# Kernel tuning notes

Measured on AMD Instinct MI355X. Metric: run time of the kernel, lower is better.

Reference implementation:

```python
import jax, jax.numpy as jnp
import numpy as np
from jax import ops

N, E, B = 50000, 800000, 64      # nodes, edges, graphs in the batch
D_RAW, D_NAMES = 48, 16          # raw node feats + name embedding -> concat = 64
HID, HEADS = 64, 4               # hidden_dim, num_heads


def setup_inputs() -> dict:
    key = jax.random.key(0)
    ks = iter(jax.random.split(key, 48))
    nrm = lambda shape, s=0.05: jax.random.normal(next(ks), shape, jnp.float32) * s
    inp = dict(
        nfeats=nrm((N, D_RAW), 1.0),
        names=nrm((N, D_NAMES), 1.0),
        centrality=jax.random.uniform(next(ks), (N, 1), jnp.float32) + 0.5,
        edge_weight=jax.random.uniform(next(ks), (E,), jnp.float32),
        src=jax.random.randint(next(ks), (E,), 0, N),
        dst=jax.random.randint(next(ks), (E,), 0, N),
        gid=jnp.sort(jax.random.randint(next(ks), (N,), 0, B)),
    )
    for l in (1, 2, 3):  # three GATConv layers (all in_feats == HID)
        inp[f'W{l}'] = nrm((HID, HEADS * HID))
        inp[f'al{l}'] = nrm((HEADS, HID))
        inp[f'ar{l}'] = nrm((HEADS, HID))
        inp[f'b{l}'] = jnp.zeros((HEADS * HID,), jnp.float32)
    for l in (0, 1, 2, 3):  # four GlobalAttentionPooling gate nets
        inp[f'Wg{l}'] = nrm((HID, 1))
        inp[f'bg{l}'] = jnp.zeros((1,), jnp.float32)
    inp['Wih'] = nrm((4 * HID, HID))
    inp['Whh'] = nrm((4 * HID, HID))
    inp['bih'] = jnp.zeros((4 * HID,), jnp.float32)
    inp['bhh'] = jnp.zeros((4 * HID,), jnp.float32)
    inp['Wc'] = nrm((HID, 1))
    inp['bc'] = jnp.zeros((1,), jnp.float32)
    return inp


def _seg_softmax(e, idx, n):
    """Numerically stable softmax of e over segments given by idx."""
    m = ops.segment_max(e, idx, num_segments=n)
    ex = jnp.exp(e - m[idx])
    s = ops.segment_sum(ex, idx, num_segments=n)
    return ex / s[idx]


def _gat(x, W, al, ar, b, src, dst, ew):
    """DGL GATConv with edge_weight: softmax over incoming edges per dst,
    edge_weight multiplied AFTER the softmax (DGL semantics), bias added."""
    n = x.shape[0]
    ft = (x @ W).reshape(n, HEADS, HID)                 # [N,H,D]
    el = jnp.einsum('nhd,hd->nh', ft, al)
    er = jnp.einsum('nhd,hd->nh', ft, ar)
    e = jax.nn.leaky_relu(el[src] + er[dst], 0.2)       # [E,H]
    a = _seg_softmax(e, dst, n) * ew[:, None]           # [E,H]
    rst = ops.segment_sum(a[:, :, None] * ft[src], dst, num_segments=n)
    return rst + b.reshape(1, HEADS, HID)               # [N,H,D]


def _gap(x, Wg, bg, gid):
    """GlobalAttentionPooling: per-graph softmax gate, weighted node sum."""
    gate = _seg_softmax(x @ Wg + bg, gid, B)            # [N,1]
    return ops.segment_sum(gate * x, gid, num_segments=B)  # [B,D]


def _lstm(xs, Wih, Whh, bih, bhh):
    h = jnp.zeros((xs.shape[1], HID), xs.dtype)
    c = h
    def step(carry, x):
        h, c = carry
        g = x @ Wih.T + bih + h @ Whh.T + bhh
        i, f, gg, o = jnp.split(g, 4, axis=-1)          # torch gate order i,f,g,o
        c = jax.nn.sigmoid(f) * c + jax.nn.sigmoid(i) * jnp.tanh(gg)
        h = jax.nn.sigmoid(o) * jnp.tanh(c)
        return (h, c), h
    (h, _), _ = jax.lax.scan(step, (h, c), xs)
    return h                                            # last hidden state [B,D]


def reference(nfeats, names, centrality, edge_weight, src, dst, gid,
              W1, al1, ar1, b1, W2, al2, ar2, b2, W3, al3, ar3, b3,
              Wg0, bg0, Wg1, bg1, Wg2, bg2, Wg3, bg3,
              Wih, Whh, bih, bhh, Wc, bc):
    x = jnp.concatenate((nfeats, names), axis=1) * centrality
    hg0 = _gap(x, Wg0, bg0, gid)
    h = jax.nn.relu(_gat(x, W1, al1, ar1, b1, src, dst, edge_weight)).mean(axis=1)
    hg1 = _gap(h, Wg1, bg1, gid)
    h = jax.nn.relu(_gat(h, W2, al2, ar2, b2, src, dst, edge_weight)).mean(axis=1)
    hg2 = _gap(h, Wg2, bg2, gid)
    h = jax.nn.relu(_gat(h, W3, al3, ar3, b3, src, dst, edge_weight)).mean(axis=1)
    hg3 = _gap(h, Wg3, bg3, gid)
    seq = jnp.stack((hg0, hg1, hg2, hg3), axis=0)       # [4,B,D]
    hT = _lstm(seq, Wih, Whh, bih, bhh)                 # [B,D]
    return jax.nn.sigmoid(hT @ Wc + bc)                 # [B,1]
```

## Files before the change

### kernel.cpp

```cpp
#include <hip/hip_runtime.h>
#include <hip/hip_bf16.h>

#define N_NODES 50000
#define N_EDGES 800000
#define N_GRAPHS 64
#define SCAN_B 196
#define FT_B   3125
#define GAP_B  512
#define G1     784
#define EPB    1024

typedef unsigned short u16;
typedef unsigned char u8;
typedef unsigned int u32;
typedef short s16x8 __attribute__((ext_vector_type(8)));
typedef float f32x4 __attribute__((ext_vector_type(4)));
typedef float f32x2 __attribute__((ext_vector_type(2)));

__device__ __forceinline__ float bf2f(u16 u) {
    union { unsigned int i; float f; } v; v.i = ((unsigned int)u) << 16; return v.f;
}
__device__ __forceinline__ u16 f2bf(float f) {
    union { float f; unsigned int i; } v; v.f = f;
    unsigned int i = v.i;
    unsigned int r = i + 0x7fffu + ((i >> 16) & 1u);
    return (u16)(r >> 16);
}
__device__ __forceinline__ float asfloat(unsigned int u) {
    union { unsigned int i; float f; } v; v.i = u; return v.f;
}

__global__ __launch_bounds__(256) void k_init(const float* __restrict__ nf, const float* __restrict__ nm,
                                              const float* __restrict__ cent, const float* __restrict__ Wg,
                                              const float* __restrict__ bg,
                                              u16* __restrict__ x, float* __restrict__ g) {
    int node = blockIdx.x * 4 + (threadIdx.x >> 6);
    int lane = threadIdx.x & 63;
    float v = (lane < 48) ? nf[(size_t)node * 48 + lane] : nm[(size_t)node * 16 + lane - 48];
    float xf = v * cent[node];
    x[(size_t)node * 64 + lane] = f2bf(xf);
    float p = xf * Wg[lane];
#pragma unroll
    for (int mm = 1; mm < 64; mm <<= 1) p += __shfl_xor(p, mm);
    if (lane == 0) g[node] = p + bg[0];
}

__global__ __launch_bounds__(256) void k_bin1(const int* __restrict__ src, const int* __restrict__ dst,
                                              const float* __restrict__ ew,
                                              u32* __restrict__ bedge, u8* __restrict__ bdlo,
                                              int* __restrict__ runstart) {
    int s = blockIdx.x, t = threadIdx.x;
    int e0 = s * EPB;
    int n = N_EDGES - e0; if (n > EPB) n = EPB; if (n < 0) n = 0;
    __shared__ int lcnt[256];
    __shared__ int lcur[256];
    __shared__ int wsum[4];
    lcnt[t] = 0;
    __syncthreads();
    for (int i = t; i < n; i += 256) atomicAdd(&lcnt[dst[e0 + i] >> 8], 1);
    __syncthreads();
    int v = lcnt[t], orig = v;
    int lane = t & 63, w = t >> 6;
#pragma unroll
    for (int d = 1; d < 64; d <<= 1) {
        int u = __shfl_up(v, d);
        if (lane >= d) v += u;
    }
    if (lane == 63) wsum[w] = v;
    __syncthreads();
    int add = 0;
    for (int k = 0; k < w; k++) add += wsum[k];
    v += add;
    int excl = v - orig;
    if (t < SCAN_B) runstart[s * 197 + t] = excl;
    if (t == 255) runstart[s * 197 + 196] = v;
    lcur[t] = excl;
    __syncthreads();
    for (int i = t; i < n; i += 256) {
        int d = dst[e0 + i];
        int pos = atomicAdd(&lcur[d >> 8], 1);
        bedge[e0 + pos] = ((u32)f2bf(ew[e0 + i]) << 16) | (u32)src[e0 + i];
        bdlo[e0 + pos] = (u8)(d & 255);
    }
}

__global__ __launch_bounds__(256) void k_cntscan(const int* __restrict__ runstart, const u8* __restrict__ bdlo,
                                                 int* __restrict__ rowptr, int* __restrict__ bsum) {
    int b = blockIdx.x, t = threadIdx.x;
    __shared__ int ndeg[256];
    __shared__ int wsum[4];
    ndeg[t] = 0;
    __syncthreads();
    for (int s = t; s < G1; s += 256) {
        int rs = runstart[s * 197 + b], re = runstart[s * 197 + b + 1];
        const u8* p = bdlo + (size_t)s * EPB;
        for (int i = rs; i < re; i++) atomicAdd(&ndeg[p[i]], 1);
    }
    __syncthreads();
    int v = ndeg[t], orig = v;
    int lane = t & 63, w = t >> 6;
#pragma unroll
    for (int d = 1; d < 64; d <<= 1) {
        int u = __shfl_up(v, d);
        if (lane >= d) v += u;
    }
    if (lane == 63) wsum[w] = v;
    __syncthreads();
    int add = 0;
    for (int k = 0; k < w; k++) add += wsum[k];
    v += add;
    int node = b * 256 + t;
    if (node < N_NODES) rowptr[node] = v - orig;
    if (t == 255) bsum[b] = v;
}

__global__ __launch_bounds__(256) void k_scanBprep(const int* __restrict__ bsum, int* __restrict__ boff,
                                                   int* __restrict__ rowptr,
                                                   const float* __restrict__ W1, const float* __restrict__ W2,
                                                   const float* __restrict__ W3, u16* __restrict__ Wt) {
    __shared__ float tile[64][65];
    __shared__ int wsum[4];
    if (blockIdx.x == 0) {
        int t = threadIdx.x;
        int v = (t < SCAN_B) ? bsum[t] : 0;
        int orig = v;
        int lane = t & 63, w = t >> 6;
#pragma unroll
        for (int d = 1; d < 64; d <<= 1) {
            int u = __shfl_up(v, d);
            if (lane >= d) v += u;
        }
        if (lane == 63) wsum[w] = v;
        __syncthreads();
        int add = 0;
        for (int k = 0; k < w; k++) add += wsum[k];
        v += add;
        if (t < SCAN_B) boff[t] = v - orig;
        if (t == 0) rowptr[N_NODES] = N_EDGES;
        return;
    }
    int bb = blockIdx.x - 1;
    int l = bb >> 2, ti = bb & 3;
    const float* W = (l == 0) ? W1 : (l == 1) ? W2 : W3;
    u16* o = Wt + (size_t)l * 64 * 256;
    int t = threadIdx.x;
    for (int i = t; i < 64 * 64; i += 256) {
        int d = i >> 6, c = i & 63;
        tile[d][c] = W[d * 256 + ti * 64 + c];
    }
    __syncthreads();
    for (int i = t; i < 64 * 64; i += 256) {
        int c = i >> 6, d = i & 63;
        o[(size_t)(ti * 64 + c) * 64 + d] = f2bf(tile[d][c]);
    }
}

__global__ __launch_bounds__(256) void k_csr2(int* __restrict__ rowptr, const int* __restrict__ boff,
                                              const int* __restrict__ runstart, const u32* __restrict__ bedge,
                                              const u8* __restrict__ bdlo, u32* __restrict__ csr_se) {
    int b = blockIdx.x, t = threadIdx.x;
    __shared__ int cur[256];
    int node = b * 256 + t;
    if (node < N_NODES) {
        int val = rowptr[node] + boff[b];
        rowptr[node] = val;
        cur[t] = val;
    } else cur[t] = 0;
    __syncthreads();
    for (int s = t; s < G1; s += 256) {
        int rs = runstart[s * 197 + b], re = runstart[s * 197 + b + 1];
        const u32* pe = bedge + (size_t)s * EPB;
        const u8* pd = bdlo + (size_t)s * EPB;
        for (int i = rs; i < re; i++) {
            int pos = atomicAdd(&cur[pd[i]], 1);
            csr_se[pos] = pe[i];
        }
    }
}

__device__ __forceinline__ void gap_part(int pb, const u16* __restrict__ x, const float* __restrict__ g,
                                         const int* __restrict__ gid,
                                         float* __restrict__ pnum, float* __restrict__ pden) {
    int part = pb & 7, b = pb >> 3;
    int t = threadIdx.x, w = t >> 6, lane = t & 63, q = lane >> 4, c = lane & 15;
    int lo = 0, hi = N_NODES;
    while (lo < hi) { int mid = (lo + hi) >> 1; if (gid[mid] < b) lo = mid + 1; else hi = mid; }
    int s = lo;
    lo = 0; hi = N_NODES;
    while (lo < hi) { int mid = (lo + hi) >> 1; if (gid[mid] < b + 1) lo = mid + 1; else hi = mid; }
    int e = lo;
    int len = e - s;
    int ps = s + (int)(((long long)len * part) >> 3);
    int pe = s + (int)(((long long)len * (part + 1)) >> 3);

    float a0 = 0.f, a1 = 0.f, a2 = 0.f, a3 = 0.f, den = 0.f;
    for (int n0 = ps + w * 4; n0 < pe; n0 += 16) {
        int node = n0 + q;
        if (node < pe) {
            float gate = __expf(fminf(g[node], 30.f));
            uint2 raw = *(const uint2*)(x + (size_t)node * 64 + c * 4);
            a0 = fmaf(gate, asfloat(raw.x << 16), a0);
            a1 = fmaf(gate, asfloat(raw.x & 0xffff0000u), a1);
            a2 = fmaf(gate, asfloat(raw.y << 16), a2);
            a3 = fmaf(gate, asfloat(raw.y & 0xffff0000u), a3);
            if (c == 0) den += gate;
        }
    }
#pragma unroll
    for (int mm = 16; mm < 64; mm <<= 1) {
        a0 += __shfl_xor(a0, mm); a1 += __shfl_xor(a1, mm);
        a2 += __shfl_xor(a2, mm); a3 += __shfl_xor(a3, mm);
        den += __shfl_xor(den, mm);
    }
    __shared__ float snum[4][64];
    __shared__ float sden[4];
    if (lane < 16) {
        snum[w][c * 4 + 0] = a0; snum[w][c * 4 + 1] = a1;
        snum[w][c * 4 + 2] = a2; snum[w][c * 4 + 3] = a3;
        if (lane == 0) sden[w] = den;
    }
    __syncthreads();
    if (t < 64) pnum[((size_t)b * 8 + part) * 64 + t] = snum[0][t] + snum[1][t] + snum[2][t] + snum[3][t];
    if (t == 0) pden[b * 8 + part] = sden[0] + sden[1] + sden[2] + sden[3];
}

__global__ __launch_bounds__(256) void k_ftgap(const u16* __restrict__ X, const u16* __restrict__ Wt,
                                               const float* __restrict__ al, const float* __restrict__ ar,
                                               u8* __restrict__ ft, float* __restrict__ el, float* __restrict__ er,
                                               const float* __restrict__ g, const int* __restrict__ gid,
                                               float* __restrict__ pnum, float* __restrict__ pden) {
    if (blockIdx.x >= FT_B) {
        gap_part(blockIdx.x - FT_B, X, g, gid, pnum, pden);
        return;
    }
    int w = threadIdx.x >> 6;
    int lane = threadIdx.x & 63;
    int quad = lane >> 4, c = lane & 15;
    int n0 = blockIdx.x * 16;

    f32x4 acc[4];
#pragma unroll
    for (int t = 0; t < 4; t++) acc[t] = (f32x4){0.f, 0.f, 0.f, 0.f};

#pragma unroll
    for (int kh = 0; kh < 2; kh++) {
        s16x8 a = *(const s16x8*)(X + (size_t)(n0 + c) * 64 + kh * 32 + quad * 8);
#pragma unroll
        for (int t = 0; t < 4; t++) {
            int col = w * 64 + t * 16 + c;
            s16x8 b = *(const s16x8*)(Wt + (size_t)col * 64 + kh * 32 + quad * 8);
            acc[t] = __builtin_amdgcn_mfma_f32_16x16x32_bf16(a, b, acc[t], 0, 0, 0);
        }
    }

    __shared__ u8 sft[16 * 256];
    float alv[4], arv[4];
#pragma unroll
    for (int t = 0; t < 4; t++) {
        alv[t] = al[w * 64 + t * 16 + c];
        arv[t] = ar[w * 64 + t * 16 + c];
    }
    float pel[4] = {0.f, 0.f, 0.f, 0.f}, per[4] = {0.f, 0.f, 0.f, 0.f};
#pragma unroll
    for (int t = 0; t < 4; t++) {
#pragma unroll
        for (int r = 0; r < 4; r++) {
            float v = acc[t][r];
            int nl = quad * 4 + r;
            int d = t * 16 + c;
            int pk = __builtin_amdgcn_cvt_pk_fp8_f32(v, v, 0, false);
            sft[nl * 256 + d * 4 + w] = (u8)(pk & 0xff);
            pel[r] += v * alv[t];
            per[r] += v * arv[t];
        }
    }
#pragma unroll
    for (int r = 0; r < 4; r++) {
#pragma unroll
        for (int mm = 1; mm < 16; mm <<= 1) {
            pel[r] += __shfl_xor(pel[r], mm);
            per[r] += __shfl_xor(per[r], mm);
        }
    }
    if (c == 0) {
#pragma unroll
        for (int r = 0; r < 4; r++) {
            int node = n0 + quad * 4 + r;
            el[node * 4 + w] = pel[r];
            er[node * 4 + w] = per[r];
        }
    }
    __syncthreads();
    const uint4* s4 = (const uint4*)sft;
    uint4* g4 = (uint4*)(ft + (size_t)n0 * 256);
    g4[threadIdx.x] = s4[threadIdx.x];
}

__global__ __launch_bounds__(256) void k_agg(
    const u8* __restrict__ ft, const float4* __restrict__ el4, const float4* __restrict__ er4,
    const int* __restrict__ rowptr, const u32* __restrict__ csr_se,
    const float* __restrict__ bias, const float* __restrict__ Wg, const float* __restrict__ bg,
    u16* __restrict__ hout, float* __restrict__ gout) {
    int wv = threadIdx.x >> 6;
    int node = blockIdx.x * 4 + wv;
    int lane = threadIdx.x & 63;
    int beg = rowptr[node], end = rowptr[node + 1];
    float4 erv = er4[node];

    __shared__ int    s_off[4][64];
    __shared__ float4 s_p[4][64];

    float S0 = 0.f, S1 = 0.f, S2 = 0.f, S3 = 0.f;
    float a0 = 0.f, a1 = 0.f, a2 = 0.f, a3 = 0.f;

    const char* ftl = (const char*)ft + lane * 4;

    for (int base = beg; base < end; base += 64) {
        int cnt = end - base; if (cnt > 64) cnt = 64;
        if (lane < cnt) {
            u32 se = csr_se[base + lane];
            int sidx = (int)(se & 0xffffu);
            float w = bf2f((u16)(se >> 16));
            float4 elv = el4[sidx];
            float t0 = elv.x + erv.x, t1 = elv.y + erv.y, t2 = elv.z + erv.z, t3 = elv.w + erv.w;
            t0 = t0 > 0.f ? t0 : 0.2f * t0;
            t1 = t1 > 0.f ? t1 : 0.2f * t1;
            t2 = t2 > 0.f ? t2 : 0.2f * t2;
            t3 = t3 > 0.f ? t3 : 0.2f * t3;
            float p0 = __expf(fminf(t0, 30.f));
            float p1 = __expf(fminf(t1, 30.f));
            float p2 = __expf(fminf(t2, 30.f));
            float p3 = __expf(fminf(t3, 30.f));
            S0 += p0; S1 += p1; S2 += p2; S3 += p3;
            s_off[wv][lane] = sidx * 256;
            s_p[wv][lane] = make_float4(p0 * w, p1 * w, p2 * w, p3 * w);
        }
        int k = 0;
        for (; k + 4 <= cnt; k += 4) {
            int o0 = s_off[wv][k], o1 = s_off[wv][k + 1], o2 = s_off[wv][k + 2], o3 = s_off[wv][k + 3];
            unsigned r0 = *(const unsigned*)(ftl + o0);
            unsigned r1 = *(const unsigned*)(ftl + o1);
            unsigned r2 = *(const unsigned*)(ftl + o2);
            unsigned r3 = *(const unsigned*)(ftl + o3);
            float4 q0 = s_p[wv][k], q1 = s_p[wv][k + 1], q2 = s_p[wv][k + 2], q3 = s_p[wv][k + 3];
            f32x2 l0 = __builtin_amdgcn_cvt_pk_f32_fp8(r0, false), h0 = __builtin_amdgcn_cvt_pk_f32_fp8(r0, true);
            f32x2 l1 = __builtin_amdgcn_cvt_pk_f32_fp8(r1, false), h1 = __builtin_amdgcn_cvt_pk_f32_fp8(r1, true);
            f32x2 l2 = __builtin_amdgcn_cvt_pk_f32_fp8(r2, false), h2 = __builtin_amdgcn_cvt_pk_f32_fp8(r2, true);
            f32x2 l3 = __builtin_amdgcn_cvt_pk_f32_fp8(r3, false), h3 = __builtin_amdgcn_cvt_pk_f32_fp8(r3, true);
            a0 = fmaf(q0.x, l0.x, a0); a1 = fmaf(q0.y, l0.y, a1);
            a2 = fmaf(q0.z, h0.x, a2); a3 = fmaf(q0.w, h0.y, a3);
            a0 = fmaf(q1.x, l1.x, a0); a1 = fmaf(q1.y, l1.y, a1);
            a2 = fmaf(q1.z, h1.x, a2); a3 = fmaf(q1.w, h1.y, a3);
            a0 = fmaf(q2.x, l2.x, a0); a1 = fmaf(q2.y, l2.y, a1);
            a2 = fmaf(q2.z, h2.x, a2); a3 = fmaf(q2.w, h2.y, a3);
            a0 = fmaf(q3.x, l3.x, a0); a1 = fmaf(q3.y, l3.y, a1);
            a2 = fmaf(q3.z, h3.x, a2); a3 = fmaf(q3.w, h3.y, a3);
        }
        for (; k < cnt; k++) {
            int o0 = s_off[wv][k];
            float4 q0 = s_p[wv][k];
            unsigned r0 = *(const unsigned*)(ftl + o0);
            f32x2 l0 = __builtin_amdgcn_cvt_pk_f32_fp8(r0, false), h0 = __builtin_amdgcn_cvt_pk_f32_fp8(r0, true);
            a0 = fmaf(q0.x, l0.x, a0); a1 = fmaf(q0.y, l0.y, a1);
            a2 = fmaf(q0.z, h0.x, a2); a3 = fmaf(q0.w, h0.y, a3);
        }
    }
#pragma unroll
    for (int mm = 1; mm < 64; mm <<= 1) {
        S0 += __shfl_xor(S0, mm);
        S1 += __shfl_xor(S1, mm);
        S2 += __shfl_xor(S2, mm);
        S3 += __shfl_xor(S3, mm);
    }
    float i0 = S0 > 0.f ? 1.f / S0 : 0.f;
    float i1 = S1 > 0.f ? 1.f / S1 : 0.f;
    float i2 = S2 > 0.f ? 1.f / S2 : 0.f;
    float i3 = S3 > 0.f ? 1.f / S3 : 0.f;
    float r0 = a0 * i0 + bias[lane];
    float r1 = a1 * i1 + bias[64 + lane];
    float r2 = a2 * i2 + bias[128 + lane];
    float r3 = a3 * i3 + bias[192 + lane];
    float o = (fmaxf(r0, 0.f) + fmaxf(r1, 0.f) + fmaxf(r2, 0.f) + fmaxf(r3, 0.f)) * 0.25f;
    hout[(size_t)node * 64 + lane] = f2bf(o);
    float pg = o * Wg[lane];
#pragma unroll
    for (int mm = 1; mm < 64; mm <<= 1) pg += __shfl_xor(pg, mm);
    if (lane == 0) gout[node] = pg + bg[0];
}

__global__ __launch_bounds__(256) void k_gapP(const u16* __restrict__ x, const float* __restrict__ g,
                                              const int* __restrict__ gid,
                                              float* __restrict__ pnum, float* __restrict__ pden) {
    gap_part(blockIdx.x, x, g, gid, pnum, pden);
}

__global__ __launch_bounds__(256) void k_lstm(const float* __restrict__ pnum, const float* __restrict__ pden,
                                              const float* __restrict__ Wih, const float* __restrict__ Whh,
                                              const float* __restrict__ bih, const float* __restrict__ bhh,
                                              const float* __restrict__ Wc, const float* __restrict__ bc,
                                              float* __restrict__ out) {
    int b = blockIdx.x, t = threadIdx.x;
    __shared__ float h[64], c[64], G[256], xv[64], red[64];
    if (t < 64) { h[t] = 0.f; c[t] = 0.f; }
    __syncthreads();
    for (int step = 0; step < 4; step++) {
        if (t < 64) {
            const float* pn = pnum + (((size_t)step * N_GRAPHS + b) * 8) * 64;
            const float* pd = pden + ((size_t)step * N_GRAPHS + b) * 8;
            float num = 0.f, dn = 0.f;
#pragma unroll
            for (int pp = 0; pp < 8; pp++) { num += pn[pp * 64 + t]; dn += pd[pp]; }
            xv[t] = (dn > 0.f) ? num / dn : 0.f;
        }
        __syncthreads();
        float acc = bih[t] + bhh[t];
#pragma unroll 4
        for (int d = 0; d < 64; d++)
            acc += xv[d] * Wih[t * 64 + d] + h[d] * Whh[t * 64 + d];
        G[t] = acc;
        __syncthreads();
        if (t < 64) {
            float ig = 1.f / (1.f + __expf(-G[t]));
            float fg = 1.f / (1.f + __expf(-G[64 + t]));
            float gg = tanhf(G[128 + t]);
            float og = 1.f / (1.f + __expf(-G[192 + t]));
            float cn = fg * c[t] + ig * gg;
            c[t] = cn;
            h[t] = og * tanhf(cn);
        }
        __syncthreads();
    }
    if (t < 64) red[t] = h[t] * Wc[t];
    __syncthreads();
    if (t == 0) {
        float r = 0.f;
        for (int i = 0; i < 64; i++) r += red[i];
        r += bc[0];
        out[b] = 1.f / (1.f + __expf(-r));
    }
}

extern "C" void kernel_launch(void* const* d_in, const int* in_sizes, int n_in,
                              void* d_out, int out_size, void* d_ws, size_t ws_size,
                              hipStream_t stream) {
    const float* nf   = (const float*)d_in[0];
    const float* nm   = (const float*)d_in[1];
    const float* cent = (const float*)d_in[2];
    const float* ew   = (const float*)d_in[3];
    const int* src  = (const int*)d_in[4];
    const int* dst  = (const int*)d_in[5];
    const int* gid  = (const int*)d_in[6];
    const float* W[3]  = {(const float*)d_in[7],  (const float*)d_in[11], (const float*)d_in[15]};
    const float* al[3] = {(const float*)d_in[8],  (const float*)d_in[12], (const float*)d_in[16]};
    const float* ar[3] = {(const float*)d_in[9],  (const float*)d_in[13], (const float*)d_in[17]};
    const float* bb[3] = {(const float*)d_in[10], (const float*)d_in[14], (const float*)d_in[18]};
    const float* Wg[4] = {(const float*)d_in[19], (const float*)d_in[21], (const float*)d_in[23], (const float*)d_in[25]};
    const float* bg[4] = {(const float*)d_in[20], (const float*)d_in[22], (const float*)d_in[24], (const float*)d_in[26]};
    const float* Wih = (const float*)d_in[27];
    const float* Whh = (const float*)d_in[28];
    const float* bih = (const float*)d_in[29];
    const float* bhh = (const float*)d_in[30];
    const float* Wc  = (const float*)d_in[31];
    const float* bc  = (const float*)d_in[32];
    float* out = (float*)d_out;

    char* p = (char*)d_ws;
    size_t off = 0;
    auto A = [&](size_t bytes) -> char* {
        char* r = p + off;
        off += (bytes + 255) & ~(size_t)255;
        return r;
    };
    u8*    ftb     = (u8*)   A((size_t)N_NODES * 256);
    u16*   nodebuf = (u16*)  A((size_t)N_NODES * 64 * 2);
    u32*   csr_se  = (u32*)  A((size_t)N_EDGES * 4);
    u32*   bedge   = (u32*)  A((size_t)G1 * EPB * 4);
    u8*    bdlo    = (u8*)   A((size_t)G1 * EPB);
    int*   runstart= (int*)  A((size_t)G1 * 197 * 4);
    float* el      = (float*)A((size_t)N_NODES * 4 * 4);
    float* er      = (float*)A((size_t)N_NODES * 4 * 4);
    float* gbuf    = (float*)A((size_t)N_NODES * 4);
    int*   rowptr  = (int*)  A((size_t)(N_NODES + 1) * 4);
    float* pnum    = (float*)A((size_t)4 * N_GRAPHS * 8 * 64 * 4);
    float* pden    = (float*)A((size_t)4 * N_GRAPHS * 8 * 4);
    int*   bsum    = (int*)  A((size_t)SCAN_B * 4);
    int*   boff    = (int*)  A((size_t)SCAN_B * 4);
    u16*   Wt      = (u16*)  A((size_t)3 * 64 * 256 * 2);

    k_init<<<N_NODES / 4, 256, 0, stream>>>(nf, nm, cent, Wg[0], bg[0], nodebuf, gbuf);
    k_bin1<<<G1, 256, 0, stream>>>(src, dst, ew, bedge, bdlo, runstart);
    k_cntscan<<<SCAN_B, 256, 0, stream>>>(runstart, bdlo, rowptr, bsum);
    k_scanBprep<<<13, 256, 0, stream>>>(bsum, boff, rowptr, W[0], W[1], W[2], Wt);
    k_csr2<<<SCAN_B, 256, 0, stream>>>(rowptr, boff, runstart, bedge, bdlo, csr_se);

    for (int l = 0; l < 3; l++) {
        k_ftgap<<<FT_B + GAP_B, 256, 0, stream>>>(nodebuf, Wt + (size_t)l * 64 * 256, al[l], ar[l],
                                                  ftb, el, er, gbuf, gid,
                                                  pnum + (size_t)l * N_GRAPHS * 8 * 64,
                                                  pden + (size_t)l * N_GRAPHS * 8);
        k_agg<<<N_NODES / 4, 256, 0, stream>>>(ftb, (const float4*)el, (const float4*)er, rowptr,
                                               csr_se, bb[l], Wg[l + 1], bg[l + 1], nodebuf, gbuf);
    }
    k_gapP<<<GAP_B, 256, 0, stream>>>(nodebuf, gbuf, gid,
                                      pnum + (size_t)3 * N_GRAPHS * 8 * 64,
                                      pden + (size_t)3 * N_GRAPHS * 8);
    k_lstm<<<N_GRAPHS, 256, 0, stream>>>(pnum, pden, Wih, Whh, bih, bhh, Wc, bc, out);
}
```

Measured before the change: 388.5 us.

## Aggregate raw node features before projection and fold attention vectors into weights

Uses linearity to reorder each GAT layer. Edges now aggregate 64-dim fp8 node inputs with per-head weights, and the 64x256 projection runs afterwards on the aggregated [N,256] result in a fused MFMA GEMM that also applies bias, relu, head mean, gate and next-layer el/er. This shrinks the gathered row from 256 bytes to 64 bytes, and el/er come from precomputed W·al and W·ar vectors. It also merges edge binning with weight prep and writes a bf16 [N,256] intermediate, which adds extra memory traffic and per-lane byte gathers.

```diff
diff --git a/kernel.cpp b/kernel.cpp
--- a/kernel.cpp
+++ b/kernel.cpp
@@ -5,7 +5,8 @@
 #define N_EDGES 800000
 #define N_GRAPHS 64
 #define SCAN_B 196
-#define FT_B   3125
+#define AGG_B  12500
+#define GEMM_B 3125
 #define GAP_B  512
 #define G1     784
 #define EPB    1024
@@ -29,58 +30,132 @@
 __device__ __forceinline__ float asfloat(unsigned int u) {
     union { unsigned int i; float f; } v; v.i = u; return v.f;
 }
+__device__ __forceinline__ u8 f2fp8(float f) {
+    int pk = __builtin_amdgcn_cvt_pk_fp8_f32(f, f, 0, false);
+    return (u8)(pk & 0xff);
+}
+__device__ __forceinline__ float fp82f(u32 b) {
+    f32x2 v = __builtin_amdgcn_cvt_pk_f32_fp8(b, false);
+    return v.x;
+}
+
+__global__ __launch_bounds__(256) void k_binprep(
+    const int* __restrict__ src, const int* __restrict__ dst, const float* __restrict__ ew,
+    u32* __restrict__ bedge, u8* __restrict__ bdlo, int* __restrict__ runstart,
+    const float* __restrict__ W1, const float* __restrict__ W2, const float* __restrict__ W3,
+    const float* __restrict__ al1, const float* __restrict__ al2, const float* __restrict__ al3,
+    const float* __restrict__ ar1, const float* __restrict__ ar2, const float* __restrict__ ar3,
+    const float* __restrict__ Wg0, const float* __restrict__ Wg1,
+    const float* __restrict__ Wg2, const float* __restrict__ Wg3,
+    u16* __restrict__ Wt, float* __restrict__ U) {
+    __shared__ float tile[64][65];
+    __shared__ int lcnt[256];
+    __shared__ int lcur[256];
+    __shared__ int wsum[4];
+    int t = threadIdx.x;
+    if (blockIdx.x < G1) {
+        int s = blockIdx.x;
+        int e0 = s * EPB;
+        int n = N_EDGES - e0; if (n > EPB) n = EPB; if (n < 0) n = 0;
+        lcnt[t] = 0;
+        __syncthreads();
+        for (int i = t; i < n; i += 256) atomicAdd(&lcnt[dst[e0 + i] >> 8], 1);
+        __syncthreads();
+        int v = lcnt[t], orig = v;
+        int lane = t & 63, w = t >> 6;
+#pragma unroll
+        for (int d = 1; d < 64; d <<= 1) {
+            int u = __shfl_up(v, d);
+            if (lane >= d) v += u;
+        }
+        if (lane == 63) wsum[w] = v;
+        __syncthreads();
+        int add = 0;
+        for (int k = 0; k < w; k++) add += wsum[k];
+        v += add;
+        int excl = v - orig;
+        if (t < SCAN_B) runstart[s * 197 + t] = excl;
+        if (t == 255) runstart[s * 197 + 196] = v;
+        lcur[t] = excl;
+        __syncthreads();
+        for (int i = t; i < n; i += 256) {
+            int d = dst[e0 + i];
+            int pos = atomicAdd(&lcur[d >> 8], 1);
+            bedge[e0 + pos] = ((u32)f2bf(ew[e0 + i]) << 16) | (u32)src[e0 + i];
+            bdlo[e0 + pos] = (u8)(d & 255);
+        }
+        return;
+    }
+    int pb = blockIdx.x - G1;
+    if (pb < 12) {
+        int l = pb >> 2, ti = pb & 3;
+        const float* W = (l == 0) ? W1 : (l == 1) ? W2 : W3;
+        u16* o = Wt + (size_t)l * 64 * 256;
+        for (int i = t; i < 64 * 64; i += 256) {
+            int d = i >> 6, c = i & 63;
+            tile[d][c] = W[d * 256 + ti * 64 + c];
+        }
+        __syncthreads();
+        for (int i = t; i < 64 * 64; i += 256) {
+            int c = i >> 6, d = i & 63;
+            o[(size_t)(ti * 64 + c) * 64 + d] = f2bf(tile[d][c]);
+        }
+        return;
+    }
+    int d = t & 63, h = t >> 6;
+    const float* Ws[3] = {W1, W2, W3};
+    const float* als[3] = {al1, al2, al3};
+    const float* ars[3] = {ar1, ar2, ar3};
+    for (int i = 0; i < 3; i++) {
+        float sa = 0.f, sr = 0.f;
+        const float* W = Ws[i];
+        const float* alp = als[i];
+        const float* arp = ars[i];
+        for (int dd = 0; dd < 64; dd++) {
+            float wv = W[d * 256 + h * 64 + dd];
+            sa += wv * alp[h * 64 + dd];
+            sr += wv * arp[h * 64 + dd];
+        }
+        U[i * 576 + (1 + h) * 64 + d] = sa;
+        U[i * 576 + (5 + h) * 64 + d] = sr;
+    }
+    if (h == 0) {
+        U[0 * 576 + d] = Wg0[d];
+        U[1 * 576 + d] = Wg1[d];
+        U[2 * 576 + d] = Wg2[d];
+        U[3 * 576 + d] = Wg3[d];
+    }
+}
 
 __global__ __launch_bounds__(256) void k_init(const float* __restrict__ nf, const float* __restrict__ nm,
-                                              const float* __restrict__ cent, const float* __restrict__ Wg,
-                                              const float* __restrict__ bg,
-                                              u16* __restrict__ x, float* __restrict__ g) {
-    int node = blockIdx.x * 4 + (threadIdx.x >> 6);
-    int lane = threadIdx.x & 63;
+                                              const float* __restrict__ cent, const float* __restrict__ U,
+                                              const float* __restrict__ bgp,
+                                              u16* __restrict__ x, u8* __restrict__ xq, float* __restrict__ g,
+                                              float* __restrict__ el, float* __restrict__ er) {
+    __shared__ float om[4][64];
+    int t = threadIdx.x;
+    int node = blockIdx.x * 4 + (t >> 6);
+    int lane = t & 63;
     float v = (lane < 48) ? nf[(size_t)node * 48 + lane] : nm[(size_t)node * 16 + lane - 48];
     float xf = v * cent[node];
     x[(size_t)node * 64 + lane] = f2bf(xf);
-    float p = xf * Wg[lane];
-#pragma unroll
-    for (int mm = 1; mm < 64; mm <<= 1) p += __shfl_xor(p, mm);
-    if (lane == 0) g[node] = p + bg[0];
-}
-
-__global__ __launch_bounds__(256) void k_bin1(const int* __restrict__ src, const int* __restrict__ dst,
-                                              const float* __restrict__ ew,
-                                              u32* __restrict__ bedge, u8* __restrict__ bdlo,
-                                              int* __restrict__ runstart) {
-    int s = blockIdx.x, t = threadIdx.x;
-    int e0 = s * EPB;
-    int n = N_EDGES - e0; if (n > EPB) n = EPB; if (n < 0) n = 0;
-    __shared__ int lcnt[256];
-    __shared__ int lcur[256];
-    __shared__ int wsum[4];
-    lcnt[t] = 0;
-    __syncthreads();
-    for (int i = t; i < n; i += 256) atomicAdd(&lcnt[dst[e0 + i] >> 8], 1);
-    __syncthreads();
-    int v = lcnt[t], orig = v;
-    int lane = t & 63, w = t >> 6;
-#pragma unroll
-    for (int d = 1; d < 64; d <<= 1) {
-        int u = __shfl_up(v, d);
-        if (lane >= d) v += u;
-    }
-    if (lane == 63) wsum[w] = v;
-    __syncthreads();
-    int add = 0;
-    for (int k = 0; k < w; k++) add += wsum[k];
-    v += add;
-    int excl = v - orig;
-    if (t < SCAN_B) runstart[s * 197 + t] = excl;
-    if (t == 255) runstart[s * 197 + 196] = v;
-    lcur[t] = excl;
-    __syncthreads();
-    for (int i = t; i < n; i += 256) {
-        int d = dst[e0 + i];
-        int pos = atomicAdd(&lcur[d >> 8], 1);
-        bedge[e0 + pos] = ((u32)f2bf(ew[e0 + i]) << 16) | (u32)src[e0 + i];
-        bdlo[e0 + pos] = (u8)(d & 255);
+    xq[(size_t)node * 64 + lane] = f2fp8(xf);
+    om[t >> 6][lane] = xf;
+    __syncthreads();
+    int j = t >> 4, nl = t & 15;
+    if (j < 9 && nl < 4) {
+        const float* u = U + j * 64;
+        float s = 0.f;
+#pragma unroll
+        for (int d4 = 0; d4 < 64; d4 += 4) {
+            float4 ov = *(const float4*)&om[nl][d4];
+            float4 uv = *(const float4*)&u[d4];
+            s += ov.x * uv.x + ov.y * uv.y + ov.z * uv.z + ov.w * uv.w;
+        }
+        int n2 = blockIdx.x * 4 + nl;
+        if (j == 0) g[n2] = s + bgp[0];
+        else if (j < 5) el[n2 * 4 + (j - 1)] = s;
+        else er[n2 * 4 + (j - 5)] = s;
     }
 }
 
@@ -114,45 +189,25 @@
     if (t == 255) bsum[b] = v;
 }
 
-__global__ __launch_bounds__(256) void k_scanBprep(const int* __restrict__ bsum, int* __restrict__ boff,
-                                                   int* __restrict__ rowptr,
-                                                   const float* __restrict__ W1, const float* __restrict__ W2,
-                                                   const float* __restrict__ W3, u16* __restrict__ Wt) {
-    __shared__ float tile[64][65];
+__global__ __launch_bounds__(256) void k_scanB(const int* __restrict__ bsum, int* __restrict__ boff,
+                                               int* __restrict__ rowptr) {
     __shared__ int wsum[4];
-    if (blockIdx.x == 0) {
-        int t = threadIdx.x;
-        int v = (t < SCAN_B) ? bsum[t] : 0;
-        int orig = v;
-        int lane = t & 63, w = t >> 6;
-#pragma unroll
-        for (int d = 1; d < 64; d <<= 1) {
-            int u = __shfl_up(v, d);
-            if (lane >= d) v += u;
-        }
-        if (lane == 63) wsum[w] = v;
-        __syncthreads();
-        int add = 0;
-        for (int k = 0; k < w; k++) add += wsum[k];
-        v += add;
-        if (t < SCAN_B) boff[t] = v - orig;
-        if (t == 0) rowptr[N_NODES] = N_EDGES;
-        return;
-    }
-    int bb = blockIdx.x - 1;
-    int l = bb >> 2, ti = bb & 3;
-    const float* W = (l == 0) ? W1 : (l == 1) ? W2 : W3;
-    u16* o = Wt + (size_t)l * 64 * 256;
     int t = threadIdx.x;
-    for (int i = t; i < 64 * 64; i += 256) {
-        int d = i >> 6, c = i & 63;
-        tile[d][c] = W[d * 256 + ti * 64 + c];
-    }
-    __syncthreads();
-    for (int i = t; i < 64 * 64; i += 256) {
-        int c = i >> 6, d = i & 63;
-        o[(size_t)(ti * 64 + c) * 64 + d] = f2bf(tile[d][c]);
-    }
+    int v = (t < SCAN_B) ? bsum[t] : 0;
+    int orig = v;
+    int lane = t & 63, w = t >> 6;
+#pragma unroll
+    for (int d = 1; d < 64; d <<= 1) {
+        int u = __shfl_up(v, d);
+        if (lane >= d) v += u;
+    }
+    if (lane == 63) wsum[w] = v;
+    __syncthreads();
+    int add = 0;
+    for (int k = 0; k < w; k++) add += wsum[k];
+    v += add;
+    if (t < SCAN_B) boff[t] = v - orig;
+    if (t == 0) rowptr[N_NODES] = N_EDGES;
 }
 
 __global__ __launch_bounds__(256) void k_csr2(int* __restrict__ rowptr, const int* __restrict__ boff,
@@ -224,96 +279,26 @@
     if (t == 0) pden[b * 8 + part] = sden[0] + sden[1] + sden[2] + sden[3];
 }
 
-__global__ __launch_bounds__(256) void k_ftgap(const u16* __restrict__ X, const u16* __restrict__ Wt,
-                                               const float* __restrict__ al, const float* __restrict__ ar,
-                                               u8* __restrict__ ft, float* __restrict__ el, float* __restrict__ er,
-                                               const float* __restrict__ g, const int* __restrict__ gid,
-                                               float* __restrict__ pnum, float* __restrict__ pden) {
-    if (blockIdx.x >= FT_B) {
-        gap_part(blockIdx.x - FT_B, X, g, gid, pnum, pden);
+__global__ __launch_bounds__(256) void k_agg(
+    const u8* __restrict__ xq, const float4* __restrict__ el4, const float4* __restrict__ er4,
+    const int* __restrict__ rowptr, const u32* __restrict__ csr_se, u16* __restrict__ aggb,
+    const u16* __restrict__ xbf, const float* __restrict__ gbuf, const int* __restrict__ gid,
+    float* __restrict__ pnum, float* __restrict__ pden) {
+    if (blockIdx.x >= AGG_B) {
+        gap_part(blockIdx.x - AGG_B, xbf, gbuf, gid, pnum, pden);
         return;
     }
-    int w = threadIdx.x >> 6;
-    int lane = threadIdx.x & 63;
-    int quad = lane >> 4, c = lane & 15;
-    int n0 = blockIdx.x * 16;
-
-    f32x4 acc[4];
-#pragma unroll
-    for (int t = 0; t < 4; t++) acc[t] = (f32x4){0.f, 0.f, 0.f, 0.f};
-
-#pragma unroll
-    for (int kh = 0; kh < 2; kh++) {
-        s16x8 a = *(const s16x8*)(X + (size_t)(n0 + c) * 64 + kh * 32 + quad * 8);
-#pragma unroll
-        for (int t = 0; t < 4; t++) {
-            int col = w * 64 + t * 16 + c;
-            s16x8 b = *(const s16x8*)(Wt + (size_t)col * 64 + kh * 32 + quad * 8);
-            acc[t] = __builtin_amdgcn_mfma_f32_16x16x32_bf16(a, b, acc[t], 0, 0, 0);
-        }
-    }
-
-    __shared__ u8 sft[16 * 256];
-    float alv[4], arv[4];
-#pragma unroll
-    for (int t = 0; t < 4; t++) {
-        alv[t] = al[w * 64 + t * 16 + c];
-        arv[t] = ar[w * 64 + t * 16 + c];
-    }
-    float pel[4] = {0.f, 0.f, 0.f, 0.f}, per[4] = {0.f, 0.f, 0.f, 0.f};
-#pragma unroll
-    for (int t = 0; t < 4; t++) {
-#pragma unroll
-        for (int r = 0; r < 4; r++) {
-            float v = acc[t][r];
-            int nl = quad * 4 + r;
-            int d = t * 16 + c;
-            int pk = __builtin_amdgcn_cvt_pk_fp8_f32(v, v, 0, false);
-            sft[nl * 256 + d * 4 + w] = (u8)(pk & 0xff);
-            pel[r] += v * alv[t];
-            per[r] += v * arv[t];
-        }
-    }
-#pragma unroll
-    for (int r = 0; r < 4; r++) {
-#pragma unroll
-        for (int mm = 1; mm < 16; mm <<= 1) {
-            pel[r] += __shfl_xor(pel[r], mm);
-            per[r] += __shfl_xor(per[r], mm);
-        }
-    }
-    if (c == 0) {
-#pragma unroll
-        for (int r = 0; r < 4; r++) {
-            int node = n0 + quad * 4 + r;
-            el[node * 4 + w] = pel[r];
-            er[node * 4 + w] = per[r];
-        }
-    }
-    __syncthreads();
-    const uint4* s4 = (const uint4*)sft;
-    uint4* g4 = (uint4*)(ft + (size_t)n0 * 256);
-    g4[threadIdx.x] = s4[threadIdx.x];
-}
-
-__global__ __launch_bounds__(256) void k_agg(
-    const u8* __restrict__ ft, const float4* __restrict__ el4, const float4* __restrict__ er4,
-    const int* __restrict__ rowptr, const u32* __restrict__ csr_se,
-    const float* __restrict__ bias, const float* __restrict__ Wg, const float* __restrict__ bg,
-    u16* __restrict__ hout, float* __restrict__ gout) {
     int wv = threadIdx.x >> 6;
     int node = blockIdx.x * 4 + wv;
     int lane = threadIdx.x & 63;
     int beg = rowptr[node], end = rowptr[node + 1];
     float4 erv = er4[node];
 
-    __shared__ int    s_off[4][64];
-    __shared__ float4 s_p[4][64];
+    __shared__ uint4 s_pk[4][64];
 
     float S0 = 0.f, S1 = 0.f, S2 = 0.f, S3 = 0.f;
     float a0 = 0.f, a1 = 0.f, a2 = 0.f, a3 = 0.f;
-
-    const char* ftl = (const char*)ft + lane * 4;
+    const u8* xl = xq + lane;
 
     for (int base = beg; base < end; base += 64) {
         int cnt = end - base; if (cnt > 64) cnt = 64;
@@ -332,37 +317,43 @@
             float p2 = __expf(fminf(t2, 30.f));
             float p3 = __expf(fminf(t3, 30.f));
             S0 += p0; S1 += p1; S2 += p2; S3 += p3;
-            s_off[wv][lane] = sidx * 256;
-            s_p[wv][lane] = make_float4(p0 * w, p1 * w, p2 * w, p3 * w);
+            p0 *= w; p1 *= w; p2 *= w; p3 *= w;
+            uint4 pk;
+            pk.x = (u32)sidx * 64;
+            pk.y = ((u32)f2bf(p1) << 16) | (u32)f2bf(p0);
+            pk.z = ((u32)f2bf(p3) << 16) | (u32)f2bf(p2);
+            pk.w = 0;
+            s_pk[wv][lane] = pk;
         }
         int k = 0;
         for (; k + 4 <= cnt; k += 4) {
-            int o0 = s_off[wv][k], o1 = s_off[wv][k + 1], o2 = s_off[wv][k + 2], o3 = s_off[wv][k + 3];
-            unsigned r0 = *(const unsigned*)(ftl + o0);
-            unsigned r1 = *(const unsigned*)(ftl + o1);
-            unsigned r2 = *(const unsigned*)(ftl + o2);
-            unsigned r3 = *(const unsigned*)(ftl + o3);
-            float4 q0 = s_p[wv][k], q1 = s_p[wv][k + 1], q2 = s_p[wv][k + 2], q3 = s_p[wv][k + 3];
-            f32x2 l0 = __builtin_amdgcn_cvt_pk_f32_fp8(r0, false), h0 = __builtin_amdgcn_cvt_pk_f32_fp8(r0, true);
-            f32x2 l1 = __builtin_amdgcn_cvt_pk_f32_fp8(r1, false), h1 = __builtin_amdgcn_cvt_pk_f32_fp8(r1, true);
-            f32x2 l2 = __builtin_amdgcn_cvt_pk_f32_fp8(r2, false), h2 = __builtin_amdgcn_cvt_pk_f32_fp8(r2, true);
-            f32x2 l3 = __builtin_amdgcn_cvt_pk_f32_fp8(r3, false), h3 = __builtin_amdgcn_cvt_pk_f32_fp8(r3, true);
-            a0 = fmaf(q0.x, l0.x, a0); a1 = fmaf(q0.y, l0.y, a1);
-            a2 = fmaf(q0.z, h0.x, a2); a3 = fmaf(q0.w, h0.y, a3);
-            a0 = fmaf(q1.x, l1.x, a0); a1 = fmaf(q1.y, l1.y, a1);
-            a2 = fmaf(q1.z, h1.x, a2); a3 = fmaf(q1.w, h1.y, a3);
-            a0 = fmaf(q2.x, l2.x, a0); a1 = fmaf(q2.y, l2.y, a1);
-            a2 = fmaf(q2.z, h2.x, a2); a3 = fmaf(q2.w, h2.y, a3);
-            a0 = fmaf(q3.x, l3.x, a0); a1 = fmaf(q3.y, l3.y, a1);
-            a2 = fmaf(q3.z, h3.x, a2); a3 = fmaf(q3.w, h3.y, a3);
+            uint4 q0 = s_pk[wv][k], q1 = s_pk[wv][k + 1], q2 = s_pk[wv][k + 2], q3 = s_pk[wv][k + 3];
+            u32 b0 = xl[q0.x], b1 = xl[q1.x], b2 = xl[q2.x], b3 = xl[q3.x];
+            float f0 = fp82f(b0), f1 = fp82f(b1), f2 = fp82f(b2), f3 = fp82f(b3);
+            a0 = fmaf(bf2f((u16)q0.y), f0, a0);
+            a1 = fmaf(bf2f((u16)(q0.y >> 16)), f0, a1);
+            a2 = fmaf(bf2f((u16)q0.z), f0, a2);
+            a3 = fmaf(bf2f((u16)(q0.z >> 16)), f0, a3);
+            a0 = fmaf(bf2f((u16)q1.y), f1, a0);
+            a1 = fmaf(bf2f((u16)(q1.y >> 16)), f1, a1);
+            a2 = fmaf(bf2f((u16)q1.z), f1, a2);
+            a3 = fmaf(bf2f((u16)(q1.z >> 16)), f1, a3);
+            a0 = fmaf(bf2f((u16)q2.y), f2, a0);
+            a1 = fmaf(bf2f((u16)(q2.y >> 16)), f2, a1);
+            a2 = fmaf(bf2f((u16)q2.z), f2, a2);
+            a3 = fmaf(bf2f((u16)(q2.z >> 16)), f2, a3);
+            a0 = fmaf(bf2f((u16)q3.y), f3, a0);
+            a1 = fmaf(bf2f((u16)(q3.y >> 16)), f3, a1);
+            a2 = fmaf(bf2f((u16)q3.z), f3, a2);
+            a3 = fmaf(bf2f((u16)(q3.z >> 16)), f3, a3);
         }
         for (; k < cnt; k++) {
-            int o0 = s_off[wv][k];
-            float4 q0 = s_p[wv][k];
-            unsigned r0 = *(const unsigned*)(ftl + o0);
-            f32x2 l0 = __builtin_amdgcn_cvt_pk_f32_fp8(r0, false), h0 = __builtin_amdgcn_cvt_pk_f32_fp8(r0, true);
-            a0 = fmaf(q0.x, l0.x, a0); a1 = fmaf(q0.y, l0.y, a1);
-            a2 = fmaf(q0.z, h0.x, a2); a3 = fmaf(q0.w, h0.y, a3);
+            uint4 q0 = s_pk[wv][k];
+            float f0 = fp82f((u32)xl[q0.x]);
+            a0 = fmaf(bf2f((u16)q0.y), f0, a0);
+            a1 = fmaf(bf2f((u16)(q0.y >> 16)), f0, a1);
+            a2 = fmaf(bf2f((u16)q0.z), f0, a2);
+            a3 = fmaf(bf2f((u16)(q0.z >> 16)), f0, a3);
         }
     }
 #pragma unroll
@@ -376,16 +367,78 @@
     float i1 = S1 > 0.f ? 1.f / S1 : 0.f;
     float i2 = S2 > 0.f ? 1.f / S2 : 0.f;
     float i3 = S3 > 0.f ? 1.f / S3 : 0.f;
-    float r0 = a0 * i0 + bias[lane];
-    float r1 = a1 * i1 + bias[64 + lane];
-    float r2 = a2 * i2 + bias[128 + lane];
-    float r3 = a3 * i3 + bias[192 + lane];
-    float o = (fmaxf(r0, 0.f) + fmaxf(r1, 0.f) + fmaxf(r2, 0.f) + fmaxf(r3, 0.f)) * 0.25f;
-    hout[(size_t)node * 64 + lane] = f2bf(o);
-    float pg = o * Wg[lane];
-#pragma unroll
-    for (int mm = 1; mm < 64; mm <<= 1) pg += __shfl_xor(pg, mm);
-    if (lane == 0) gout[node] = pg + bg[0];
+    size_t base = (size_t)node * 256;
+    aggb[base + lane]       = f2bf(a0 * i0);
+    aggb[base + 64 + lane]  = f2bf(a1 * i1);
+    aggb[base + 128 + lane] = f2bf(a2 * i2);
+    aggb[base + 192 + lane] = f2bf(a3 * i3);
+}
+
+__global__ __launch_bounds__(256) void k_gemm(const u16* __restrict__ aggb, const u16* __restrict__ Wt,
+                                              const float* __restrict__ bias, const float* __restrict__ U,
+                                              const float* __restrict__ bgp, int last,
+                                              u16* __restrict__ xbf, u8* __restrict__ xq,
+                                              float* __restrict__ gbuf,
+                                              float* __restrict__ el, float* __restrict__ er) {
+    int w = threadIdx.x >> 6;
+    int lane = threadIdx.x & 63;
+    int quad = lane >> 4, c = lane & 15;
+    int n0 = blockIdx.x * 16;
+
+    f32x4 acc[4];
+#pragma unroll
+    for (int t = 0; t < 4; t++) acc[t] = (f32x4){0.f, 0.f, 0.f, 0.f};
+
+#pragma unroll
+    for (int kh = 0; kh < 2; kh++) {
+        s16x8 a = *(const s16x8*)(aggb + (size_t)(n0 + c) * 256 + w * 64 + kh * 32 + quad * 8);
+#pragma unroll
+        for (int t = 0; t < 4; t++) {
+            int col = w * 64 + t * 16 + c;
+            s16x8 b = *(const s16x8*)(Wt + (size_t)col * 64 + kh * 32 + quad * 8);
+            acc[t] = __builtin_amdgcn_mfma_f32_16x16x32_bf16(a, b, acc[t], 0, 0, 0);
+        }
+    }
+
+    __shared__ float sf[4][16][64];
+    __shared__ float om[16][64];
+#pragma unroll
+    for (int t = 0; t < 4; t++) {
+#pragma unroll
+        for (int r = 0; r < 4; r++) {
+            int d = t * 16 + c;
+            int nl = quad * 4 + r;
+            sf[w][nl][d] = fmaxf(acc[t][r] + bias[w * 64 + d], 0.f);
+        }
+    }
+    __syncthreads();
+    int t = threadIdx.x;
+    int d = t & 63, wg = t >> 6;
+#pragma unroll
+    for (int i = 0; i < 4; i++) {
+        int nl = i * 4 + wg;
+        int node = n0 + nl;
+        float o = 0.25f * (sf[0][nl][d] + sf[1][nl][d] + sf[2][nl][d] + sf[3][nl][d]);
+        om[nl][d] = o;
+        xbf[(size_t)node * 64 + d] = f2bf(o);
+        xq[(size_t)node * 64 + d] = f2fp8(o);
+    }
+    __syncthreads();
+    int j = t >> 4, nl2 = t & 15;
+    if (j < 9 && !(last && j > 0)) {
+        const float* u = U + j * 64;
+        float s = 0.f;
+#pragma unroll
+        for (int d4 = 0; d4 < 64; d4 += 4) {
+            float4 ov = *(const float4*)&om[nl2][d4];
+            float4 uv = *(const float4*)&u[d4];
+            s += ov.x * uv.x + ov.y * uv.y + ov.z * uv.z + ov.w * uv.w;
+        }
+        int node = n0 + nl2;
+        if (j == 0) gbuf[node] = s + bgp[0];
+        else if (j < 5) el[node * 4 + (j - 1)] = s;
+        else er[node * 4 + (j - 5)] = s;
+    }
 }
 
 __global__ __launch_bounds__(256) void k_gapP(const u16* __restrict__ x, const float* __restrict__ g,
@@ -471,8 +524,9 @@
         off += (bytes + 255) & ~(size_t)255;
         return r;
     };
-    u8*    ftb     = (u8*)   A((size_t)N_NODES * 256);
-    u16*   nodebuf = (u16*)  A((size_t)N_NODES * 64 * 2);
+    u16*   aggb    = (u16*)  A((size_t)N_NODES * 256 * 2);
+    u16*   xbf     = (u16*)  A((size_t)N_NODES * 64 * 2);
+    u8*    xq      = (u8*)   A((size_t)N_NODES * 64);
     u32*   csr_se  = (u32*)  A((size_t)N_EDGES * 4);
     u32*   bedge   = (u32*)  A((size_t)G1 * EPB * 4);
     u8*    bdlo    = (u8*)   A((size_t)G1 * EPB);
@@ -486,22 +540,26 @@
     int*   bsum    = (int*)  A((size_t)SCAN_B * 4);
     int*   boff    = (int*)  A((size_t)SCAN_B * 4);
     u16*   Wt      = (u16*)  A((size_t)3 * 64 * 256 * 2);
-
-    k_init<<<N_NODES / 4, 256, 0, stream>>>(nf, nm, cent, Wg[0], bg[0], nodebuf, gbuf);
-    k_bin1<<<G1, 256, 0, stream>>>(src, dst, ew, bedge, bdlo, runstart);
+    float* U       = (float*)A((size_t)4 * 9 * 64 * 4);
+
+    k_binprep<<<G1 + 13, 256, 0, stream>>>(src, dst, ew, bedge, bdlo, runstart,
+                                           W[0], W[1], W[2], al[0], al[1], al[2], ar[0], ar[1], ar[2],
+                                           Wg[0], Wg[1], Wg[2], Wg[3], Wt, U);
+    k_init<<<AGG_B, 256, 0, stream>>>(nf, nm, cent, U, bg[0], xbf, xq, gbuf, el, er);
     k_cntscan<<<SCAN_B, 256, 0, stream>>>(runstart, bdlo, rowptr, bsum);
-    k_scanBprep<<<13, 256, 0, stream>>>(bsum, boff, rowptr, W[0], W[1], W[2], Wt);
+    k_scanB<<<1, 256, 0, stream>>>(bsum, boff, rowptr);
     k_csr2<<<SCAN_B, 256, 0, stream>>>(rowptr, boff, runstart, bedge, bdlo, csr_se);
 
     for (int l = 0; l < 3; l++) {
-        k_ftgap<<<FT_B + GAP_B, 256, 0, stream>>>(nodebuf, Wt + (size_t)l * 64 * 256, al[l], ar[l],
-                                                  ftb, el, er, gbuf, gid,
-                                                  pnum + (size_t)l * N_GRAPHS * 8 * 64,
-                                                  pden + (size_t)l * N_GRAPHS * 8);
-        k_agg<<<N_NODES / 4, 256, 0, stream>>>(ftb, (const float4*)el, (const float4*)er, rowptr,
-                                               csr_se, bb[l], Wg[l + 1], bg[l + 1], nodebuf, gbuf);
-    }
-    k_gapP<<<GAP_B, 256, 0, stream>>>(nodebuf, gbuf, gid,
+        k_agg<<<AGG_B + GAP_B, 256, 0, stream>>>(xq, (const float4*)el, (const float4*)er, rowptr,
+                                                 csr_se, aggb, xbf, gbuf, gid,
+                                                 pnum + (size_t)l * N_GRAPHS * 8 * 64,
+                                                 pden + (size_t)l * N_GRAPHS * 8);
+        k_gemm<<<GEMM_B, 256, 0, stream>>>(aggb, Wt + (size_t)l * 64 * 256, bb[l],
+                                           U + (size_t)(l + 1) * 576, bg[l + 1], (l == 2) ? 1 : 0,
+                                           xbf, xq, gbuf, el, er);
+    }
+    k_gapP<<<GAP_B, 256, 0, stream>>>(xbf, gbuf, gid,
                                       pnum + (size_t)3 * N_GRAPHS * 8 * 64,
                                       pden + (size_t)3 * N_GRAPHS * 8);
     k_lstm<<<N_GRAPHS, 256, 0, stream>>>(pnum, pden, Wih, Whh, bih, bhh, Wc, bc, out);
```

New measurement: 407.9 us. +5.0%, slower.
